# Kernel tuning notes

Hardware: AMD Instinct MI355X
Metric: run time of the kernel (lower is better)

## Reference

```python
import jax, jax.numpy as jnp
import numpy as np

L, D, H, KVH, DH, F, V, SMAX, T = 4, 2048, 16, 8, 128, 6144, 32000, 2048, 1024
EPS = 1e-6
ROPE_THETA = 1e6


def rotate_half(x, axis=-1):
    x1, x2 = jnp.split(x, 2, axis=axis)
    return jnp.concatenate((-x2, x1), axis=axis)


def rms(x, w):
    return w * (x / jnp.sqrt(jnp.mean(x * x, axis=-1, keepdims=True) + EPS))


def setup_inputs() -> dict:
    key = jax.random.key(0)
    ks = jax.random.split(key, 16)
    s = 0.02
    inv_freq = 1.0 / (ROPE_THETA ** (jnp.arange(0, DH, 2, dtype=jnp.float32) / DH))
    ang = jnp.arange(SMAX, dtype=jnp.float32)[:, None] * inv_freq[None, :]  # [SMAX, DH/2]
    cos_emb = jnp.concatenate([jnp.cos(ang), jnp.cos(ang)], axis=-1)  # [SMAX, DH]
    sin_emb = jnp.concatenate([jnp.sin(ang), jnp.sin(ang)], axis=-1)
    sf = DH ** (-0.25)  # scale_factor pre-baked into q_norm/k_norm weights
    return {
        "key_buffer": jnp.zeros((L, KVH, 1, DH, SMAX), jnp.float32),
        "value_buffer": jnp.zeros((L, KVH, 1, SMAX, DH), jnp.float32),
        "input_ids": jax.random.randint(ks[0], (1, T), 0, V, dtype=jnp.int32),
        "attention_mask": jnp.ones((1, T, T), jnp.float32),
        "past_len": 0,
        "embed_data": jax.random.randint(ks[1], (V, D), 0, 256).astype(jnp.uint8),
        "embed_scale": jax.random.uniform(ks[2], (V, 1), jnp.float32, 0.001, 0.02),
        "embed_zero": jax.random.normal(ks[3], (V, 1), jnp.float32) * 0.1,
        "cos_emb": cos_emb,
        "sin_emb": sin_emb,
        "w_in_ln": jnp.ones((L, D), jnp.float32),
        "Wq": jax.random.normal(ks[4], (L, D, H * DH), jnp.float32) * s,
        "Wk": jax.random.normal(ks[5], (L, D, KVH * DH), jnp.float32) * s,
        "Wv": jax.random.normal(ks[6], (L, D, KVH * DH), jnp.float32) * s,
        "w_q_norm": jnp.full((L, DH), sf, jnp.float32),
        "w_k_norm": jnp.full((L, DH), sf, jnp.float32),
        "Wo": jax.random.normal(ks[7], (L, H * DH, D), jnp.float32) * s,
        "w_post_ln": jnp.ones((L, D), jnp.float32),
        "Wgate": jax.random.normal(ks[8], (L, D, F), jnp.float32) * s,
        "Wup": jax.random.normal(ks[9], (L, D, F), jnp.float32) * s,
        "Wdown": jax.random.normal(ks[10], (L, F, D), jnp.float32) * s,
        "w_final_norm": jnp.ones((D,), jnp.float32),
        "W_lm": jax.random.normal(ks[11], (D, V), jnp.float32) * s,
    }


def reference(key_buffer, value_buffer, input_ids, attention_mask, past_len,
              embed_data, embed_scale, embed_zero, cos_emb, sin_emb,
              w_in_ln, Wq, Wk, Wv, w_q_norm, w_k_norm, Wo, w_post_ln,
              Wgate, Wup, Wdown, w_final_norm, W_lm):
    new_len = input_ids.shape[1]
    end = past_len + new_len  # static (past_len is a Python int)
    cos_q = cos_emb[past_len:end]  # [T, DH]
    sin_q = sin_emb[past_len:end]
    # uint8 embedding dequant: e * scale + zero_point
    hidden = embed_data[input_ids].astype(jnp.float32) * embed_scale[input_ids] + embed_zero[input_ids]  # [1,T,D]
    # causal mask: (1 - tril) * -128, sliced to [1, new_len, end], times user mask
    rows = jnp.arange(new_len) + past_len
    cols = jnp.arange(end)
    mask = jnp.where(cols[None, :] <= rows[:, None], 0.0, -128.0)[None] * attention_mask  # [1,T,end]
    G = H // KVH
    for i in range(L):
        hn = rms(hidden, w_in_ln[i])[0]  # [T, D]
        q = (hn @ Wq[i]).reshape(new_len, H, DH)
        q = jnp.transpose(rms(q, w_q_norm[i]), (1, 0, 2))  # [H,T,DH] (sqrt(scale) baked in w_q_norm)
        k = (hn @ Wk[i]).reshape(new_len, KVH, DH)
        k = jnp.transpose(rms(k, w_k_norm[i]), (1, 2, 0))  # [KVH,DH,T]
        v = jnp.transpose((hn @ Wv[i]).reshape(new_len, KVH, DH), (1, 0, 2))  # [KVH,T,DH]
        # RoPE on keys (rotate along DH axis=1)
        k = k * cos_q.T + rotate_half(k, axis=1) * sin_q.T
        key_buffer = jax.lax.dynamic_update_slice(key_buffer, k[None, :, None], (i, 0, 0, 0, past_len))
        value_buffer = jax.lax.dynamic_update_slice(value_buffer, v[None, :, None], (i, 0, 0, past_len, 0))
        # GQA expand: each kv head repeated G times consecutively
        k_exp = jnp.repeat(key_buffer[i, :, 0, :, :end], G, axis=0)  # [H,DH,end]
        v_exp = jnp.repeat(value_buffer[i, :, 0, :end, :], G, axis=0)  # [H,end,DH]
        q_rot = q * cos_q[None] + rotate_half(q, axis=-1) * sin_q[None]
        scores = jnp.einsum('htd,hds->hts', q_rot, k_exp) + mask
        attn = jax.nn.softmax(scores, axis=-1)
        ctx = jnp.transpose(jnp.einsum('hts,hsd->htd', attn, v_exp), (1, 0, 2)).reshape(1, new_len, H * DH)
        hidden = hidden + ctx @ Wo[i]
        hn2 = rms(hidden, w_post_ln[i])
        hidden = hidden + (jax.nn.silu(hn2 @ Wgate[i]) * (hn2 @ Wup[i])) @ Wdown[i]
    last = rms(hidden[:, -1], w_final_norm)  # [1, D]
    logits = last @ W_lm  # [1, V]
    tok_id = jnp.argmax(logits, axis=-1, keepdims=True).astype(jnp.int32)
    new_seq_len = jnp.array([end], dtype=jnp.int32)
    return (tok_id, key_buffer, value_buffer, new_seq_len)
```

## Files before the change

### kernel.cpp

```cpp
#include <hip/hip_runtime.h>
#include <cstdint>

#define L_ 4
#define D_ 2048
#define H_ 16
#define KVH_ 8
#define DH_ 128
#define F_ 6144
#define V_ 32000
#define SMAX_ 2048
#define T_ 1024
#define EPS_ 1e-6f
#define QB 32
#define SB 128
#define ZSE 4194304

typedef unsigned short u16;
typedef unsigned int u32;
typedef float fvec4 __attribute__((ext_vector_type(4)));
typedef float f32x4 __attribute__((ext_vector_type(4)));
typedef __bf16 bf16x8 __attribute__((ext_vector_type(8)));

__device__ __forceinline__ u16 f2bf(float f) {
  union { float f; u32 u; } a; a.f = f;
  u32 u = a.u;
  return (u16)((u + 0x7FFFu + ((u >> 16) & 1u)) >> 16);
}
__device__ __forceinline__ float bf2f(u16 h) {
  union { u32 u; float f; } a; a.u = (u32)h << 16; return a.f;
}
__device__ __forceinline__ fvec4 bf4(uint2 u) {
  union { u32 i; float f; } a, b, c, d;
  a.i = u.x << 16; b.i = u.x & 0xFFFF0000u;
  c.i = u.y << 16; d.i = u.y & 0xFFFF0000u;
  fvec4 r; r[0] = a.f; r[1] = b.f; r[2] = c.f; r[3] = d.f; return r;
}

__device__ __forceinline__ void gld16(const void* g, void* l) {
  __builtin_amdgcn_global_load_lds(
      (const __attribute__((address_space(1))) void*)g,
      (__attribute__((address_space(3))) void*)l, 16, 0, 0);
}

__global__ void embed_k(const int* __restrict__ ids, const void* __restrict__ edata,
                        const float* __restrict__ esc, const float* __restrict__ ez,
                        float* __restrict__ hidden)
{
  const int* ei = (const int*)edata;
  int chk = ei[threadIdx.x & 63];
  bool ok = ((unsigned)chk) <= 255u;
  bool is_i32 = (__ballot(ok) == ~0ULL);
  int t = blockIdx.x;
  int id = ids[t];
  float sc = esc[id], zp = ez[id];
  size_t base = (size_t)id * D_;
  const uint8_t* eb = (const uint8_t*)edata;
  for (int d = threadIdx.x; d < D_; d += 256) {
    float e = is_i32 ? (float)ei[base + d] : (float)eb[base + d];
    hidden[(size_t)t * D_ + d] = e * sc + zp;
  }
}

__device__ __forceinline__ void convT_body(const float* __restrict__ W, int N,
                                           int nb, int kb, int K, int rb,
                                           u16* __restrict__ WT, int gu, float* tile)
{
  int n0 = nb * 64, k0 = kb * 64;
  int tid = threadIdx.x;
  int lk = tid >> 4, n4 = (tid & 15) * 4;
#pragma unroll
  for (int i = 0; i < 4; ++i) {
    int kr = i * 16 + lk;
    fvec4 v = *(const fvec4*)(W + (size_t)(k0 + kr) * N + n0 + n4);
#pragma unroll
    for (int j = 0; j < 4; ++j) tile[(n4 + j) * 65 + kr] = v[j];
  }
  __syncthreads();
  int n = tid >> 2, kq = (tid & 3) * 16;
  int f = n0 + n;
  int row = gu ? (rb + ((f >> 4) << 5) + (f & 15)) : (rb + f);
  union { u16 h[16]; uint4 q[2]; } o;
#pragma unroll
  for (int i = 0; i < 16; ++i) o.h[i] = f2bf(tile[n * 65 + kq + i]);
  u16* op = WT + (size_t)row * K + k0 + kq;
  *(uint4*)op = o.q[0];
  *(uint4*)(op + 8) = o.q[1];
}

template<int NZ>
__device__ __forceinline__ void rms_body(int idx, float* __restrict__ x,
                                         const u16* __restrict__ p,
                                         const float* __restrict__ w,
                                         u16* __restrict__ out)
{
  int t = idx * 4 + (threadIdx.x >> 6);
  int l = threadIdx.x & 63;
  fvec4* xr = (fvec4*)(x + (size_t)t * D_);
  fvec4 v[8];
#pragma unroll
  for (int j = 0; j < 8; ++j) v[j] = xr[l + 64 * j];
  if (NZ > 0) {
#pragma unroll
    for (int z = 0; z < NZ; ++z) {
      const uint2* a = (const uint2*)(p + (size_t)z * ZSE + (size_t)t * D_);
#pragma unroll
      for (int j = 0; j < 8; ++j) v[j] += bf4(a[l + 64 * j]);
    }
#pragma unroll
    for (int j = 0; j < 8; ++j) xr[l + 64 * j] = v[j];
  }
  float s = 0.f;
#pragma unroll
  for (int j = 0; j < 8; ++j)
    s += v[j][0]*v[j][0] + v[j][1]*v[j][1] + v[j][2]*v[j][2] + v[j][3]*v[j][3];
#pragma unroll
  for (int m = 32; m; m >>= 1) s += __shfl_xor(s, m);
  float inv = rsqrtf(s * (1.f / D_) + EPS_);
  const fvec4* wr = (const fvec4*)w;
  u16* orow = out + (size_t)t * D_;
#pragma unroll
  for (int j = 0; j < 8; ++j) {
    fvec4 wv = wr[l + 64 * j];
    uint2 o;
    o.x = (u32)f2bf(wv[0]*v[j][0]*inv) | ((u32)f2bf(wv[1]*v[j][1]*inv) << 16);
    o.y = (u32)f2bf(wv[2]*v[j][2]*inv) | ((u32)f2bf(wv[3]*v[j][3]*inv) << 16);
    *(uint2*)(orow + (l + 64 * j) * 4) = o;
  }
}

template<int NZ>
__global__ __launch_bounds__(256)
void convqkv_rms_k(const float* __restrict__ Wq, const float* __restrict__ Wk,
                   const float* __restrict__ Wv, u16* __restrict__ WT,
                   float* __restrict__ x, const u16* __restrict__ p,
                   const float* __restrict__ w, u16* __restrict__ out)
{
  __shared__ float tile[64 * 65];
  int bx = blockIdx.x, y = blockIdx.y;
  if (bx < 64) {
    const float* W; int N, nb, rb;
    if (bx < 32)      { W = Wq; N = 2048; nb = bx;      rb = 0; }
    else if (bx < 48) { W = Wk; N = 1024; nb = bx - 32; rb = 2048; }
    else              { W = Wv; N = 1024; nb = bx - 48; rb = 3072; }
    convT_body(W, N, nb, y, 2048, rb, WT, 0, tile);
  } else {
    rms_body<NZ>((bx - 64) * 32 + y, x, p, w, out);
  }
}

__global__ __launch_bounds__(256)
void convgu_wd_rms_k(const float* __restrict__ Wg, const float* __restrict__ Wu,
                     u16* __restrict__ WTgu, const float* __restrict__ Wd,
                     u16* __restrict__ WTwd,
                     float* __restrict__ x, const u16* __restrict__ p,
                     const float* __restrict__ w, u16* __restrict__ out)
{
  __shared__ float tile[64 * 65];
  int bx = blockIdx.x, y = blockIdx.y;
  if (bx < 192) {
    const float* W; int nb, rb;
    if (bx < 96) { W = Wg; nb = bx;      rb = 0; }
    else         { W = Wu; nb = bx - 96; rb = 16; }
    convT_body(W, 6144, nb, y, 2048, rb, WTgu, 1, tile);
  } else if (bx < 288) {
    int xp = bx - 192;
    convT_body(Wd, 2048, xp & 31, ((xp >> 5) << 5) + y, 6144, 0, WTwd, 0, tile);
  } else {
    rms_body<4>((bx - 288) * 32 + y, x, p, w, out);
  }
}

template<int EPI>
__global__ __launch_bounds__(256)
void gemm_bt(const u16* __restrict__ A, const u16* __restrict__ B,
             u16* __restrict__ Cb, int K, int Ks, int ldC, long long zStride)
{
  __shared__ u16 lA[128 * 64];
  __shared__ u16 lB[128 * 64];
  const u16* Ab = A + (size_t)blockIdx.y * 128 * K;
  const u16* Bb = B + (size_t)blockIdx.x * 128 * K;
  int kz = blockIdx.z * Ks;

  int tid = threadIdx.x;
  int l = tid & 63;
  int wid = tid >> 6;
  int wr = wid >> 1, wc = wid & 1;
  int lrow = l & 15, lk = l >> 4;

  f32x4 acc[4][4] = {};

  for (int k0 = 0; k0 < Ks; k0 += 64) {
#pragma unroll
    for (int r = 0; r < 4; ++r) {
      int c = r * 256 + tid;
      int row = c >> 3, g = c & 7;
      int kel = kz + k0 + ((g ^ (row & 7)) << 3);
      gld16(Ab + (size_t)row * K + kel, (char*)lA + c * 16);
      gld16(Bb + (size_t)row * K + kel, (char*)lB + c * 16);
    }
    __syncthreads();
#pragma unroll
    for (int kk = 0; kk < 2; ++kk) {
      bf16x8 av[4], bv[4];
      int kbyte = (kk * 32 + lk * 8) * 2;
#pragma unroll
      for (int m = 0; m < 4; ++m) {
        int row = wr * 64 + m * 16 + lrow;
        int byt = (row * 128 + kbyte) ^ ((row & 7) << 4);
        av[m] = *(const bf16x8*)((const char*)lA + byt);
      }
#pragma unroll
      for (int n = 0; n < 4; ++n) {
        int row = wc * 64 + n * 16 + lrow;
        int byt = (row * 128 + kbyte) ^ ((row & 7) << 4);
        bv[n] = *(const bf16x8*)((const char*)lB + byt);
      }
#pragma unroll
      for (int m = 0; m < 4; ++m)
#pragma unroll
        for (int n = 0; n < 4; ++n)
          acc[m][n] = __builtin_amdgcn_mfma_f32_16x16x32_bf16(av[m], bv[n], acc[m][n], 0, 0, 0);
    }
    __syncthreads();
  }

  int grow0 = blockIdx.y * 128 + wr * 64 + lk * 4;
  if (EPI == 3) {
    int fcol0 = blockIdx.x * 64 + wc * 32 + lrow;
#pragma unroll
    for (int m = 0; m < 4; ++m)
#pragma unroll
      for (int np = 0; np < 2; ++np)
#pragma unroll
        for (int r = 0; r < 4; ++r) {
          float g = acc[m][2 * np][r], u = acc[m][2 * np + 1][r];
          float val = g / (1.f + __expf(-g)) * u;
          Cb[(size_t)(grow0 + m * 16 + r) * ldC + fcol0 + np * 16] = f2bf(val);
        }
    return;
  }
  u16* Cz = Cb + (long long)blockIdx.z * zStride;
  int gcol0 = blockIdx.x * 128 + wc * 64 + lrow;
#pragma unroll
  for (int m = 0; m < 4; ++m)
#pragma unroll
    for (int n = 0; n < 4; ++n)
#pragma unroll
      for (int r = 0; r < 4; ++r)
        Cz[(size_t)(grow0 + m * 16 + r) * ldC + gcol0 + n * 16] = f2bf(acc[m][n][r]);
}

__global__ __launch_bounds__(256)
void qkvpost_convwo_k(const u16* __restrict__ p0, const u16* __restrict__ p1,
                      const float* __restrict__ wq, const float* __restrict__ wk,
                      const float* __restrict__ cosT, const float* __restrict__ sinT,
                      const int* __restrict__ plp,
                      u16* __restrict__ qr, u16* __restrict__ kr, u16* __restrict__ vT,
                      float* __restrict__ key_out, float* __restrict__ val_out,
                      const float* __restrict__ Wo, u16* __restrict__ WTo)
{
  __shared__ float tile[64][132];
  if (blockIdx.x >= 16) {
    convT_body(Wo, 2048, blockIdx.x - 16, blockIdx.y, 2048, 0, WTo, 0, &tile[0][0]);
    return;
  }
  int t0 = blockIdx.x * 64;
  int z = blockIdx.y;
  int pl = plp[0];
  int tid = threadIdx.x;
  int cb = z < 16 ? z * 128 : (z < 24 ? 2048 + (z - 16) * 128 : 3072 + (z - 24) * 128);

  {
    int r = tid >> 5;
    int c = (tid & 31) * 4;
#pragma unroll
    for (int i = 0; i < 8; ++i) {
      int row = i * 8 + r;
      size_t off = (size_t)(t0 + row) * 4096 + cb + c;
      fvec4 v = bf4(*(const uint2*)(p0 + off)) + bf4(*(const uint2*)(p1 + off));
      *(fvec4*)&tile[row][c] = v;
    }
  }
  __syncthreads();

  if (z < 24) {
    int row = tid >> 2, q = tid & 3;
    int dbase = q * 32, pbase = (q ^ 2) * 32;
    const float* wn = z < 16 ? wq : wk;
    float sgn = (q < 2) ? -1.f : 1.f;
    fvec4 xv[8];
    float ss = 0.f;
#pragma unroll
    for (int j = 0; j < 8; ++j) {
      xv[j] = *(const fvec4*)&tile[row][dbase + j * 4];
      ss += xv[j][0]*xv[j][0] + xv[j][1]*xv[j][1] + xv[j][2]*xv[j][2] + xv[j][3]*xv[j][3];
    }
    ss += __shfl_xor(ss, 1);
    ss += __shfl_xor(ss, 2);
    float inv = rsqrtf(ss * (1.f / 128.f) + EPS_);
    int p = pl + t0 + row;
    float rv[32];
#pragma unroll
    for (int j = 0; j < 8; ++j) {
      fvec4 xo = *(const fvec4*)&tile[row][pbase + j * 4];
      fvec4 wv = *(const fvec4*)(wn + dbase + j * 4);
      fvec4 wo = *(const fvec4*)(wn + pbase + j * 4);
      fvec4 cs = *(const fvec4*)(cosT + (size_t)p * 128 + dbase + j * 4);
      fvec4 sn = *(const fvec4*)(sinT + (size_t)p * 128 + dbase + j * 4);
#pragma unroll
      for (int e = 0; e < 4; ++e) {
        float xn = wv[e] * xv[j][e] * inv;
        float xp = wo[e] * xo[e] * inv;
        rv[j * 4 + e] = xn * cs[e] + sgn * xp * sn[e];
      }
    }
    union { u32 w[8]; uint4 q4[2]; } ob;
    u16* orow = (z < 16 ? qr + ((size_t)z * T_ + t0 + row) * 128
                        : kr + ((size_t)(z - 16) * T_ + t0 + row) * 128) + dbase;
#pragma unroll
    for (int j = 0; j < 8; ++j)
      ob.w[j] = (u32)f2bf(rv[2 * j]) | ((u32)f2bf(rv[2 * j + 1]) << 16);
    *(uint4*)orow = ob.q4[0];
    *(uint4*)(orow + 8) = ob.q4[1];
#pragma unroll
    for (int j = 0; j < 8; ++j)
      ob.w[j] = (u32)f2bf(rv[16 + 2 * j]) | ((u32)f2bf(rv[17 + 2 * j]) << 16);
    *(uint4*)(orow + 16) = ob.q4[0];
    *(uint4*)(orow + 24) = ob.q4[1];

    if (z >= 16) {
      __syncthreads();
#pragma unroll
      for (int j = 0; j < 8; ++j) {
        fvec4 v; v[0] = rv[j*4]; v[1] = rv[j*4+1]; v[2] = rv[j*4+2]; v[3] = rv[j*4+3];
        *(fvec4*)&tile[row][dbase + j * 4] = v;
      }
      __syncthreads();
      int d = tid >> 1, cc = (tid & 1) * 32;
      float* kp = key_out + ((size_t)(z - 16) * 128 + d) * SMAX_ + pl + t0 + cc;
      if ((pl & 3) == 0) {
#pragma unroll
        for (int j4 = 0; j4 < 8; ++j4) {
          fvec4 v;
#pragma unroll
          for (int e = 0; e < 4; ++e) v[e] = tile[cc + j4 * 4 + e][d];
          *(fvec4*)(kp + j4 * 4) = v;
        }
      } else {
        for (int j = 0; j < 32; ++j) kp[j] = tile[cc + j][d];
      }
    }
  } else {
    int kv = z - 24;
    int row = tid >> 2, q = tid & 3;
    float* vp = val_out + ((size_t)kv * SMAX_ + pl + t0 + row) * 128 + q * 32;
#pragma unroll
    for (int j = 0; j < 8; ++j)
      *(fvec4*)(vp + j * 4) = *(const fvec4*)&tile[row][q * 32 + j * 4];
    int d = tid >> 1, cc = (tid & 1) * 32;
    union { u32 w[16]; uint4 q4[4]; } ob;
    u16* tp = vT + ((size_t)kv * 128 + d) * T_ + t0 + cc;
#pragma unroll
    for (int j = 0; j < 16; ++j)
      ob.w[j] = (u32)f2bf(tile[cc + 2 * j][d]) | ((u32)f2bf(tile[cc + 2 * j + 1][d]) << 16);
    *(uint4*)tp = ob.q4[0];
    *(uint4*)(tp + 8) = ob.q4[1];
    *(uint4*)(tp + 16) = ob.q4[2];
    *(uint4*)(tp + 24) = ob.q4[3];
  }
}

__global__ __launch_bounds__(256)
void flash_k(const u16* __restrict__ qr, const u16* __restrict__ kr,
             const u16* __restrict__ vTb, const float* __restrict__ am,
             const int* __restrict__ plp, u16* __restrict__ ctx)
{
  __shared__ u16 lQ[QB * DH_];
  __shared__ u16 lKV[SB * DH_];
  __shared__ u16 lP[QB * SB];
  __shared__ float lMax[2][2][16];
  __shared__ float lSum[2][2][16];
  __shared__ float lScale[QB];
  __shared__ float lFin[QB];

  int qt = gridDim.x - 1 - blockIdx.x;
  int h = blockIdx.y;
  int kvh = h >> 1;
  int pl = plp[0];
  int tid = threadIdx.x;
  int l = tid & 63, w = tid >> 6;
  int lrow = l & 15, lk = l >> 4;
  int tb = w & 1, sh = w >> 1;
  int tcol = tb * 16 + lrow;

  const u16* Qb = qr + ((size_t)h * T_ + qt * QB) * DH_;
  const u16* Kb = kr + (size_t)kvh * T_ * DH_;
  const u16* Vb = vTb + (size_t)kvh * DH_ * T_;

#pragma unroll
  for (int r = 0; r < 2; ++r) {
    int c = r * 256 + tid;
    int row = c >> 4, g = c & 15;
    gld16(Qb + (size_t)row * DH_ + ((g ^ (row & 7)) << 3), (char*)lQ + c * 16);
  }

  float m_run = -3.0e38f, l_run = 0.f;
  f32x4 acc_o[2][2] = {};

  int t_lo = qt * QB;
  int s_hi = min(T_, t_lo + QB + pl);
  int nt = (s_hi + SB - 1) / SB;
  int tg = t_lo + tcol;

  for (int it = 0; it < nt; ++it) {
    int s0 = it * SB;
#pragma unroll
    for (int r = 0; r < 8; ++r) {
      int c = r * 256 + tid;
      int row = c >> 4, g = c & 15;
      gld16(Kb + (size_t)(s0 + row) * DH_ + ((g ^ (row & 7)) << 3), (char*)lKV + c * 16);
    }
    __syncthreads();

    f32x4 acc_s[4] = {};
#pragma unroll
    for (int kk = 0; kk < 4; ++kk) {
      int kbyte = kk * 64 + lk * 16;
      int trow = tb * 16 + lrow;
      bf16x8 bq = *(const bf16x8*)((const char*)lQ + ((trow * 256 + kbyte) ^ ((trow & 7) << 4)));
#pragma unroll
      for (int m = 0; m < 4; ++m) {
        int srow = sh * 64 + m * 16 + lrow;
        bf16x8 ak = *(const bf16x8*)((const char*)lKV + ((srow * 256 + kbyte) ^ ((srow & 7) << 4)));
        acc_s[m] = __builtin_amdgcn_mfma_f32_16x16x32_bf16(ak, bq, acc_s[m], 0, 0, 0);
      }
    }
    __syncthreads();

#pragma unroll
    for (int r = 0; r < 8; ++r) {
      int c = r * 256 + tid;
      int row = c >> 4, g = c & 15;
      gld16(Vb + (size_t)row * T_ + s0 + ((g ^ (row & 7)) << 3), (char*)lKV + c * 16);
    }

    bool full = (s0 + SB <= t_lo + pl + 1);
    float sv[4][4];
    float vmax = -3.0e38f;
    if (full) {
#pragma unroll
      for (int m = 0; m < 4; ++m)
#pragma unroll
        for (int r = 0; r < 4; ++r) {
          float val = acc_s[m][r]; sv[m][r] = val; vmax = fmaxf(vmax, val);
        }
    } else {
#pragma unroll
      for (int m = 0; m < 4; ++m) {
        int sg = s0 + sh * 64 + m * 16 + lk * 4;
        fvec4 a4 = *(const fvec4*)(am + (size_t)tg * T_ + sg);
#pragma unroll
        for (int r = 0; r < 4; ++r) {
          float val = acc_s[m][r] + ((sg + r <= tg + pl) ? 0.f : -128.f * a4[r]);
          sv[m][r] = val; vmax = fmaxf(vmax, val);
        }
      }
    }
    vmax = fmaxf(vmax, __shfl_xor(vmax, 16));
    vmax = fmaxf(vmax, __shfl_xor(vmax, 32));
    if (lk == 0) lMax[tb][sh][lrow] = vmax;
    __syncthreads();

    float om = fmaxf(lMax[tb][0][lrow], lMax[tb][1][lrow]);
    float m_new = fmaxf(m_run, om);
    float corr = __expf(m_run - m_new);
    float psum = 0.f;
    u32 pw[4][2];
#pragma unroll
    for (int m = 0; m < 4; ++m) {
      float p0 = __expf(sv[m][0] - m_new);
      float p1 = __expf(sv[m][1] - m_new);
      float p2 = __expf(sv[m][2] - m_new);
      float p3 = __expf(sv[m][3] - m_new);
      psum += (p0 + p1) + (p2 + p3);
      pw[m][0] = (u32)f2bf(p0) | ((u32)f2bf(p1) << 16);
      pw[m][1] = (u32)f2bf(p2) | ((u32)f2bf(p3) << 16);
    }
    psum += __shfl_xor(psum, 16);
    psum += __shfl_xor(psum, 32);
    if (lk == 0) lSum[tb][sh][lrow] = psum;
    if (lk == 0 && sh == 0) lScale[tcol] = corr;
#pragma unroll
    for (int m = 0; m < 4; ++m) {
      int byt = (tcol * 256 + sh * 128 + m * 32 + lk * 8) ^ ((tcol & 7) << 4);
      *(uint2*)((char*)lP + byt) = make_uint2(pw[m][0], pw[m][1]);
    }
    __syncthreads();

    l_run = l_run * corr + lSum[tb][0][lrow] + lSum[tb][1][lrow];
    m_run = m_new;
#pragma unroll
    for (int m = 0; m < 2; ++m) {
      fvec4 c4 = *(const fvec4*)&lScale[m * 16 + lk * 4];
#pragma unroll
      for (int n = 0; n < 2; ++n)
#pragma unroll
        for (int r = 0; r < 4; ++r) acc_o[m][n][r] *= c4[r];
    }
#pragma unroll
    for (int kk = 0; kk < 4; ++kk) {
      int kbyte = kk * 64 + lk * 16;
      bf16x8 ap[2], bv[2];
#pragma unroll
      for (int m = 0; m < 2; ++m) {
        int trow = m * 16 + lrow;
        ap[m] = *(const bf16x8*)((const char*)lP + ((trow * 256 + kbyte) ^ ((trow & 7) << 4)));
      }
#pragma unroll
      for (int n = 0; n < 2; ++n) {
        int drow = w * 32 + n * 16 + lrow;
        bv[n] = *(const bf16x8*)((const char*)lKV + ((drow * 256 + kbyte) ^ ((drow & 7) << 4)));
      }
#pragma unroll
      for (int m = 0; m < 2; ++m)
#pragma unroll
        for (int n = 0; n < 2; ++n)
          acc_o[m][n] = __builtin_amdgcn_mfma_f32_16x16x32_bf16(ap[m], bv[n], acc_o[m][n], 0, 0, 0);
    }
    __syncthreads();
  }

  if (lk == 0 && sh == 0) lFin[tcol] = l_run;
  __syncthreads();
#pragma unroll
  for (int m = 0; m < 2; ++m) {
    fvec4 s4 = *(const fvec4*)&lFin[m * 16 + lk * 4];
#pragma unroll
    for (int r = 0; r < 4; ++r) {
      float inv = 1.f / s4[r];
      int trow = t_lo + m * 16 + lk * 4 + r;
      u16* crow = ctx + (size_t)trow * (H_ * DH_) + h * DH_;
#pragma unroll
      for (int n = 0; n < 2; ++n) {
        int d = w * 32 + n * 16 + lrow;
        crow[d] = f2bf(acc_o[m][n][r] * inv);
      }
    }
  }
}

__global__ void frms_k(const float* __restrict__ x, const u16* __restrict__ p,
                       const float* __restrict__ w, float* __restrict__ out)
{
  __shared__ float sm[4];
  float s = 0.f;
  for (int d = threadIdx.x; d < D_; d += 256) {
    float v = x[d] + bf2f(p[d]) + bf2f(p[ZSE + d]) + bf2f(p[2 * ZSE + d]) + bf2f(p[3 * ZSE + d]);
    s += v * v;
  }
#pragma unroll
  for (int m = 32; m; m >>= 1) s += __shfl_xor(s, m);
  if ((threadIdx.x & 63) == 0) sm[threadIdx.x >> 6] = s;
  __syncthreads();
  s = sm[0] + sm[1] + sm[2] + sm[3];
  float inv = rsqrtf(s * (1.f / D_) + EPS_);
  for (int d = threadIdx.x; d < D_; d += 256)
    out[d] = w[d] * (x[d] + bf2f(p[d]) + bf2f(p[ZSE + d]) + bf2f(p[2 * ZSE + d]) + bf2f(p[3 * ZSE + d])) * inv;
}

__global__ void lmgemv_k(const float* __restrict__ last, const float* __restrict__ Wlm,
                         float* __restrict__ part)
{
  __shared__ float ls[256];
  int v = blockIdx.x * 256 + threadIdx.x;
  int c = blockIdx.y;
  ls[threadIdx.x] = last[c * 256 + threadIdx.x];
  __syncthreads();
  const float* Wp = Wlm + (size_t)c * 256 * V_ + v;
  float acc = 0.f;
#pragma unroll 8
  for (int d = 0; d < 256; d++) acc += ls[d] * Wp[(size_t)d * V_];
  part[(size_t)c * V_ + v] = acc;
}

__global__ void amax_part_k(const float* __restrict__ part, float2* __restrict__ out)
{
  __shared__ float sv[4];
  __shared__ int si[4];
  int v = blockIdx.x * 256 + threadIdx.x;
  float val = 0.f;
#pragma unroll
  for (int c = 0; c < 8; c++) val += part[(size_t)c * V_ + v];
  float bv = val; int bi = v;
#pragma unroll
  for (int m = 32; m; m >>= 1) {
    float ov = __shfl_xor(bv, m);
    int oi = __shfl_xor(bi, m);
    if (ov > bv || (ov == bv && oi < bi)) { bv = ov; bi = oi; }
  }
  if ((threadIdx.x & 63) == 0) { sv[threadIdx.x >> 6] = bv; si[threadIdx.x >> 6] = bi; }
  __syncthreads();
  if (threadIdx.x == 0) {
    for (int w = 1; w < 4; w++)
      if (sv[w] > bv || (sv[w] == bv && si[w] < bi)) { bv = sv[w]; bi = si[w]; }
    out[blockIdx.x] = make_float2(bv, (float)bi);
  }
}

__global__ void finalize_k(const float2* __restrict__ part, int np,
                           const int* __restrict__ plp, float* __restrict__ dout,
                           unsigned long long lastoff)
{
  if (threadIdx.x == 0) {
    float bv = part[0].x; int bi = (int)part[0].y;
    for (int b = 1; b < np; b++) {
      float v = part[b].x; int i = (int)part[b].y;
      if (v > bv || (v == bv && i < bi)) { bv = v; bi = i; }
    }
    dout[0] = (float)bi;
    dout[lastoff] = (float)(plp[0] + T_);
  }
}

extern "C" void kernel_launch(void* const* d_in, const int* in_sizes, int n_in,
                              void* d_out, int out_size, void* d_ws, size_t ws_size,
                              hipStream_t stream)
{
  (void)in_sizes; (void)n_in; (void)out_size; (void)ws_size;

  const float* key_in  = (const float*)d_in[0];
  const float* val_in  = (const float*)d_in[1];
  const int*   ids     = (const int*)d_in[2];
  const float* am      = (const float*)d_in[3];
  const int*   plp     = (const int*)d_in[4];
  const void*  edata   = d_in[5];
  const float* esc     = (const float*)d_in[6];
  const float* ez      = (const float*)d_in[7];
  const float* cosT    = (const float*)d_in[8];
  const float* sinT    = (const float*)d_in[9];
  const float* w_in_ln = (const float*)d_in[10];
  const float* Wq      = (const float*)d_in[11];
  const float* Wk      = (const float*)d_in[12];
  const float* Wv      = (const float*)d_in[13];
  const float* wqn     = (const float*)d_in[14];
  const float* wkn     = (const float*)d_in[15];
  const float* Wo      = (const float*)d_in[16];
  const float* wpost   = (const float*)d_in[17];
  const float* Wg      = (const float*)d_in[18];
  const float* Wu      = (const float*)d_in[19];
  const float* Wd      = (const float*)d_in[20];
  const float* wfin    = (const float*)d_in[21];
  const float* Wlm     = (const float*)d_in[22];

  float* out = (float*)d_out;
  const size_t KVN = (size_t)L_ * KVH_ * DH_ * SMAX_;
  float* key_out = out + 1;
  float* val_out = out + 1 + KVN;
  unsigned long long lastoff = 1 + 2 * KVN;

  char* ws = (char*)d_ws;
  u16*   wT     = (u16*)  (ws + 0);
  u16*   wTwd   = wT + 25165824;
  u16*   hn     = (u16*)  (ws + 75497472);
  u16*   P      = (u16*)  (ws + 79691776);
  u16*   qr     = (u16*)  (ws + 113246208);
  u16*   kr     = (u16*)  (ws + 117440512);
  u16*   vT     = (u16*)  (ws + 119537664);
  u16*   ctx    = (u16*)  (ws + 121634816);
  float* hidden = (float*)(ws + 125829120);
  u16*   mlp    = (u16*)  (ws + 134217728);
  float* last   = (float*)(ws + 146800640);
  float* lpart  = (float*)(ws + 146808832);
  float2* amaxp = (float2*)(ws + 147832832);

  hipMemcpyAsync(key_out, key_in, KVN * sizeof(float), hipMemcpyDeviceToDevice, stream);
  hipMemcpyAsync(val_out, val_in, KVN * sizeof(float), hipMemcpyDeviceToDevice, stream);
  embed_k<<<T_, 256, 0, stream>>>(ids, edata, esc, ez, hidden);

  for (int i = 0; i < L_; i++) {
    if (i == 0)
      convqkv_rms_k<0><<<dim3(72, 32), 256, 0, stream>>>(
          Wq, Wk, Wv, wT, hidden, nullptr, w_in_ln, hn);
    else
      convqkv_rms_k<4><<<dim3(72, 32), 256, 0, stream>>>(
          Wq + (size_t)i * 4194304, Wk + (size_t)i * 2097152, Wv + (size_t)i * 2097152,
          wT, hidden, P, w_in_ln + (size_t)i * D_, hn);

    gemm_bt<0><<<dim3(32, 8, 2), 256, 0, stream>>>(hn, wT, P, 2048, 1024, 4096, ZSE);

    qkvpost_convwo_k<<<dim3(48, 32), 256, 0, stream>>>(P, P + ZSE,
        wqn + (size_t)i * DH_, wkn + (size_t)i * DH_, cosT, sinT, plp,
        qr, kr, vT,
        key_out + (size_t)i * KVH_ * DH_ * SMAX_,
        val_out + (size_t)i * KVH_ * SMAX_ * DH_,
        Wo + (size_t)i * 4194304, wT);

    flash_k<<<dim3(T_ / QB, H_), 256, 0, stream>>>(qr, kr, vT, am, plp, ctx);

    gemm_bt<0><<<dim3(16, 8, 4), 256, 0, stream>>>(ctx, wT, P, 2048, 512, 2048, ZSE);

    convgu_wd_rms_k<<<dim3(296, 32), 256, 0, stream>>>(
        Wg + (size_t)i * 12582912, Wu + (size_t)i * 12582912, wT,
        Wd + (size_t)i * 12582912, wTwd,
        hidden, P, wpost + (size_t)i * D_, hn);

    gemm_bt<3><<<dim3(96, 8, 1), 256, 0, stream>>>(hn, wT, mlp, 2048, 2048, 6144, 0);

    gemm_bt<0><<<dim3(16, 8, 4), 256, 0, stream>>>(mlp, wTwd, P, 6144, 1536, 2048, ZSE);
  }

  frms_k<<<1, 256, 0, stream>>>(hidden + (size_t)(T_ - 1) * D_,
                                P + (size_t)(T_ - 1) * D_, wfin, last);
  lmgemv_k<<<dim3(V_ / 256, 8), 256, 0, stream>>>(last, Wlm, lpart);
  amax_part_k<<<V_ / 256, 256, 0, stream>>>(lpart, amaxp);
  finalize_k<<<1, 64, 0, stream>>>(amaxp, V_ / 256, plp, out, lastoff);
}
```

Measured before the change: 1.133 ms.

## Co-schedule QKV GEMM with Wo/gate/up/down weight conversion in one kernel

Moves the Wo, gate/up and down weight transpose-conversions into one grid with the QKV GEMM, so the bandwidth-bound conversion blocks overlap the compute-bound GEMM blocks. The RMSNorm that was fused with the MLP conversion becomes a standalone kernel, and the final RMS is folded into the LM-head GEMV. The workspace is re-laid out with separate buffers per converted weight and a smaller partial stride, and the mlp buffer now aliases the QKV weight area. Risks include load imbalance from the heterogeneous grid, and each LM GEMV block recomputing the final norm.

```diff
diff --git a/kernel.cpp b/kernel.cpp
--- a/kernel.cpp
+++ b/kernel.cpp
@@ -13,7 +13,8 @@
 #define EPS_ 1e-6f
 #define QB 32
 #define SB 128
-#define ZSE 4194304
+#define ZQK 4194304
+#define ZS2 2097152
 
 typedef unsigned short u16;
 typedef unsigned int u32;
@@ -89,7 +90,7 @@
 
 template<int NZ>
 __device__ __forceinline__ void rms_body(int idx, float* __restrict__ x,
-                                         const u16* __restrict__ p,
+                                         const u16* __restrict__ p, int zs,
                                          const float* __restrict__ w,
                                          u16* __restrict__ out)
 {
@@ -102,7 +103,7 @@
   if (NZ > 0) {
 #pragma unroll
     for (int z = 0; z < NZ; ++z) {
-      const uint2* a = (const uint2*)(p + (size_t)z * ZSE + (size_t)t * D_);
+      const uint2* a = (const uint2*)(p + (size_t)z * zs + (size_t)t * D_);
 #pragma unroll
       for (int j = 0; j < 8; ++j) v[j] += bf4(a[l + 64 * j]);
     }
@@ -144,42 +145,29 @@
     else              { W = Wv; N = 1024; nb = bx - 48; rb = 3072; }
     convT_body(W, N, nb, y, 2048, rb, WT, 0, tile);
   } else {
-    rms_body<NZ>((bx - 64) * 32 + y, x, p, w, out);
+    rms_body<NZ>((bx - 64) * 32 + y, x, p, ZS2, w, out);
   }
 }
 
 __global__ __launch_bounds__(256)
-void convgu_wd_rms_k(const float* __restrict__ Wg, const float* __restrict__ Wu,
-                     u16* __restrict__ WTgu, const float* __restrict__ Wd,
-                     u16* __restrict__ WTwd,
-                     float* __restrict__ x, const u16* __restrict__ p,
-                     const float* __restrict__ w, u16* __restrict__ out)
-{
-  __shared__ float tile[64 * 65];
-  int bx = blockIdx.x, y = blockIdx.y;
-  if (bx < 192) {
-    const float* W; int nb, rb;
-    if (bx < 96) { W = Wg; nb = bx;      rb = 0; }
-    else         { W = Wu; nb = bx - 96; rb = 16; }
-    convT_body(W, 6144, nb, y, 2048, rb, WTgu, 1, tile);
-  } else if (bx < 288) {
-    int xp = bx - 192;
-    convT_body(Wd, 2048, xp & 31, ((xp >> 5) << 5) + y, 6144, 0, WTwd, 0, tile);
-  } else {
-    rms_body<4>((bx - 288) * 32 + y, x, p, w, out);
-  }
+void rms_k(float* __restrict__ x, const u16* __restrict__ p,
+           const float* __restrict__ w, u16* __restrict__ out)
+{
+  rms_body<4>(blockIdx.x, x, p, ZS2, w, out);
 }
 
 template<int EPI>
-__global__ __launch_bounds__(256)
-void gemm_bt(const u16* __restrict__ A, const u16* __restrict__ B,
-             u16* __restrict__ Cb, int K, int Ks, int ldC, long long zStride)
-{
-  __shared__ u16 lA[128 * 64];
-  __shared__ u16 lB[128 * 64];
-  const u16* Ab = A + (size_t)blockIdx.y * 128 * K;
-  const u16* Bb = B + (size_t)blockIdx.x * 128 * K;
-  int kz = blockIdx.z * Ks;
+__device__ __forceinline__ void gemm_body(const u16* __restrict__ A,
+                                          const u16* __restrict__ B,
+                                          u16* __restrict__ Cb,
+                                          int K, int Ks, int ldC, long long zStride,
+                                          int bx, int by, int bz, char* smem)
+{
+  u16* lA = (u16*)smem;
+  u16* lB = (u16*)(smem + 16384);
+  const u16* Ab = A + (size_t)by * 128 * K;
+  const u16* Bb = B + (size_t)bx * 128 * K;
+  int kz = bz * Ks;
 
   int tid = threadIdx.x;
   int l = tid & 63;
@@ -224,9 +212,9 @@
     __syncthreads();
   }
 
-  int grow0 = blockIdx.y * 128 + wr * 64 + lk * 4;
+  int grow0 = by * 128 + wr * 64 + lk * 4;
   if (EPI == 3) {
-    int fcol0 = blockIdx.x * 64 + wc * 32 + lrow;
+    int fcol0 = bx * 64 + wc * 32 + lrow;
 #pragma unroll
     for (int m = 0; m < 4; ++m)
 #pragma unroll
@@ -239,8 +227,8 @@
         }
     return;
   }
-  u16* Cz = Cb + (long long)blockIdx.z * zStride;
-  int gcol0 = blockIdx.x * 128 + wc * 64 + lrow;
+  u16* Cz = Cb + (long long)bz * zStride;
+  int gcol0 = bx * 128 + wc * 64 + lrow;
 #pragma unroll
   for (int m = 0; m < 4; ++m)
 #pragma unroll
@@ -250,20 +238,52 @@
         Cz[(size_t)(grow0 + m * 16 + r) * ldC + gcol0 + n * 16] = f2bf(acc[m][n][r]);
 }
 
+template<int EPI>
 __global__ __launch_bounds__(256)
-void qkvpost_convwo_k(const u16* __restrict__ p0, const u16* __restrict__ p1,
-                      const float* __restrict__ wq, const float* __restrict__ wk,
-                      const float* __restrict__ cosT, const float* __restrict__ sinT,
-                      const int* __restrict__ plp,
-                      u16* __restrict__ qr, u16* __restrict__ kr, u16* __restrict__ vT,
-                      float* __restrict__ key_out, float* __restrict__ val_out,
-                      const float* __restrict__ Wo, u16* __restrict__ WTo)
+void gemm_bt(const u16* __restrict__ A, const u16* __restrict__ B,
+             u16* __restrict__ Cb, int K, int Ks, int ldC, long long zStride)
+{
+  __shared__ char smem[32768];
+  gemm_body<EPI>(A, B, Cb, K, Ks, ldC, zStride, blockIdx.x, blockIdx.y, blockIdx.z, smem);
+}
+
+__global__ __launch_bounds__(256)
+void qkvgemm_conv_k(const u16* __restrict__ hn, const u16* __restrict__ wTqkv,
+                    u16* __restrict__ P,
+                    const float* __restrict__ Wo, u16* __restrict__ wTo,
+                    const float* __restrict__ Wg, const float* __restrict__ Wu,
+                    u16* __restrict__ wTgu,
+                    const float* __restrict__ Wd, u16* __restrict__ wTwd)
+{
+  __shared__ char smem[32768];
+  int bx = blockIdx.x;
+  if (bx < 512) {
+    gemm_body<0>(hn, wTqkv, P, 2048, 1024, 4096, ZQK,
+                 bx & 31, (bx >> 5) & 7, bx >> 8, smem);
+  } else if (bx < 1536) {
+    int cb = bx - 512;
+    convT_body(Wo, 2048, cb & 31, cb >> 5, 2048, 0, wTo, 0, (float*)smem);
+  } else if (bx < 7680) {
+    int cb = bx - 1536;
+    int x = cb % 192, y = cb / 192;
+    const float* W = x < 96 ? Wg : Wu;
+    convT_body(W, 6144, x < 96 ? x : x - 96, y, 2048, x < 96 ? 0 : 16, wTgu, 1, (float*)smem);
+  } else {
+    int cb = bx - 7680;
+    int xp = cb % 96, y = cb / 96;
+    convT_body(Wd, 2048, xp & 31, ((xp >> 5) << 5) + y, 6144, 0, wTwd, 0, (float*)smem);
+  }
+}
+
+__global__ __launch_bounds__(256)
+void qkvpost_k(const u16* __restrict__ p0, const u16* __restrict__ p1,
+               const float* __restrict__ wq, const float* __restrict__ wk,
+               const float* __restrict__ cosT, const float* __restrict__ sinT,
+               const int* __restrict__ plp,
+               u16* __restrict__ qr, u16* __restrict__ kr, u16* __restrict__ vT,
+               float* __restrict__ key_out, float* __restrict__ val_out)
 {
   __shared__ float tile[64][132];
-  if (blockIdx.x >= 16) {
-    convT_body(Wo, 2048, blockIdx.x - 16, blockIdx.y, 2048, 0, WTo, 0, &tile[0][0]);
-    return;
-  }
   int t0 = blockIdx.x * 64;
   int z = blockIdx.y;
   int pl = plp[0];
@@ -549,33 +569,33 @@
   }
 }
 
-__global__ void frms_k(const float* __restrict__ x, const u16* __restrict__ p,
-                       const float* __restrict__ w, float* __restrict__ out)
-{
+__global__ void lmgemv_k(const float* __restrict__ x, const u16* __restrict__ p,
+                         const float* __restrict__ wfin, const float* __restrict__ Wlm,
+                         float* __restrict__ part)
+{
+  __shared__ float ls[256];
   __shared__ float sm[4];
+  int tid = threadIdx.x;
+  int c = blockIdx.y;
+  float xv[8];
   float s = 0.f;
-  for (int d = threadIdx.x; d < D_; d += 256) {
-    float v = x[d] + bf2f(p[d]) + bf2f(p[ZSE + d]) + bf2f(p[2 * ZSE + d]) + bf2f(p[3 * ZSE + d]);
-    s += v * v;
+#pragma unroll
+  for (int j = 0; j < 8; ++j) {
+    int d = j * 256 + tid;
+    float v = x[d] + bf2f(p[d]) + bf2f(p[ZS2 + d]) + bf2f(p[2 * ZS2 + d]) + bf2f(p[3 * ZS2 + d]);
+    xv[j] = v; s += v * v;
   }
 #pragma unroll
   for (int m = 32; m; m >>= 1) s += __shfl_xor(s, m);
-  if ((threadIdx.x & 63) == 0) sm[threadIdx.x >> 6] = s;
+  if ((tid & 63) == 0) sm[tid >> 6] = s;
   __syncthreads();
   s = sm[0] + sm[1] + sm[2] + sm[3];
   float inv = rsqrtf(s * (1.f / D_) + EPS_);
-  for (int d = threadIdx.x; d < D_; d += 256)
-    out[d] = w[d] * (x[d] + bf2f(p[d]) + bf2f(p[ZSE + d]) + bf2f(p[2 * ZSE + d]) + bf2f(p[3 * ZSE + d])) * inv;
-}
-
-__global__ void lmgemv_k(const float* __restrict__ last, const float* __restrict__ Wlm,
-                         float* __restrict__ part)
-{
-  __shared__ float ls[256];
-  int v = blockIdx.x * 256 + threadIdx.x;
-  int c = blockIdx.y;
-  ls[threadIdx.x] = last[c * 256 + threadIdx.x];
+#pragma unroll
+  for (int j = 0; j < 8; ++j)
+    if (j == c) ls[tid] = wfin[j * 256 + tid] * xv[j] * inv;
   __syncthreads();
+  int v = blockIdx.x * 256 + tid;
   const float* Wp = Wlm + (size_t)c * 256 * V_ + v;
   float acc = 0.f;
 #pragma unroll 8
@@ -659,19 +679,20 @@
   unsigned long long lastoff = 1 + 2 * KVN;
 
   char* ws = (char*)d_ws;
-  u16*   wT     = (u16*)  (ws + 0);
-  u16*   wTwd   = wT + 25165824;
-  u16*   hn     = (u16*)  (ws + 75497472);
-  u16*   P      = (u16*)  (ws + 79691776);
-  u16*   qr     = (u16*)  (ws + 113246208);
-  u16*   kr     = (u16*)  (ws + 117440512);
-  u16*   vT     = (u16*)  (ws + 119537664);
-  u16*   ctx    = (u16*)  (ws + 121634816);
-  float* hidden = (float*)(ws + 125829120);
-  u16*   mlp    = (u16*)  (ws + 134217728);
-  float* last   = (float*)(ws + 146800640);
-  float* lpart  = (float*)(ws + 146808832);
-  float2* amaxp = (float2*)(ws + 147832832);
+  u16*   wTqkv  = (u16*)  (ws + 0);
+  u16*   mlp    = (u16*)  (ws + 0);
+  float* lpart  = (float*)(ws + 16777216);
+  float2* amaxp = (float2*)(ws + 17825792);
+  u16*   wTo    = (u16*)  (ws + 33554432);
+  u16*   wTgu   = (u16*)  (ws + 41943040);
+  u16*   wTwd   = (u16*)  (ws + 92274688);
+  u16*   P      = (u16*)  (ws + 117440512);
+  u16*   hn     = (u16*)  (ws + 134217728);
+  u16*   qr     = (u16*)  (ws + 138412032);
+  u16*   kr     = (u16*)  (ws + 142606336);
+  u16*   vT     = (u16*)  (ws + 144703488);
+  u16*   ctx    = (u16*)  (ws + 146800640);
+  float* hidden = (float*)(ws + 150994944);
 
   hipMemcpyAsync(key_out, key_in, KVN * sizeof(float), hipMemcpyDeviceToDevice, stream);
   hipMemcpyAsync(val_out, val_in, KVN * sizeof(float), hipMemcpyDeviceToDevice, stream);
@@ -680,38 +701,37 @@
   for (int i = 0; i < L_; i++) {
     if (i == 0)
       convqkv_rms_k<0><<<dim3(72, 32), 256, 0, stream>>>(
-          Wq, Wk, Wv, wT, hidden, nullptr, w_in_ln, hn);
+          Wq, Wk, Wv, wTqkv, hidden, nullptr, w_in_ln, hn);
     else
       convqkv_rms_k<4><<<dim3(72, 32), 256, 0, stream>>>(
           Wq + (size_t)i * 4194304, Wk + (size_t)i * 2097152, Wv + (size_t)i * 2097152,
-          wT, hidden, P, w_in_ln + (size_t)i * D_, hn);
-
-    gemm_bt<0><<<dim3(32, 8, 2), 256, 0, stream>>>(hn, wT, P, 2048, 1024, 4096, ZSE);
-
-    qkvpost_convwo_k<<<dim3(48, 32), 256, 0, stream>>>(P, P + ZSE,
+          wTqkv, hidden, P, w_in_ln + (size_t)i * D_, hn);
+
+    qkvgemm_conv_k<<<10752, 256, 0, stream>>>(
+        hn, wTqkv, P,
+        Wo + (size_t)i * 4194304, wTo,
+        Wg + (size_t)i * 12582912, Wu + (size_t)i * 12582912, wTgu,
+        Wd + (size_t)i * 12582912, wTwd);
+
+    qkvpost_k<<<dim3(16, 32), 256, 0, stream>>>(P, P + ZQK,
         wqn + (size_t)i * DH_, wkn + (size_t)i * DH_, cosT, sinT, plp,
         qr, kr, vT,
         key_out + (size_t)i * KVH_ * DH_ * SMAX_,
-        val_out + (size_t)i * KVH_ * SMAX_ * DH_,
-        Wo + (size_t)i * 4194304, wT);
+        val_out + (size_t)i * KVH_ * SMAX_ * DH_);
 
     flash_k<<<dim3(T_ / QB, H_), 256, 0, stream>>>(qr, kr, vT, am, plp, ctx);
 
-    gemm_bt<0><<<dim3(16, 8, 4), 256, 0, stream>>>(ctx, wT, P, 2048, 512, 2048, ZSE);
-
-    convgu_wd_rms_k<<<dim3(296, 32), 256, 0, stream>>>(
-        Wg + (size_t)i * 12582912, Wu + (size_t)i * 12582912, wT,
-        Wd + (size_t)i * 12582912, wTwd,
-        hidden, P, wpost + (size_t)i * D_, hn);
-
-    gemm_bt<3><<<dim3(96, 8, 1), 256, 0, stream>>>(hn, wT, mlp, 2048, 2048, 6144, 0);
-
-    gemm_bt<0><<<dim3(16, 8, 4), 256, 0, stream>>>(mlp, wTwd, P, 6144, 1536, 2048, ZSE);
-  }
-
-  frms_k<<<1, 256, 0, stream>>>(hidden + (size_t)(T_ - 1) * D_,
-                                P + (size_t)(T_ - 1) * D_, wfin, last);
-  lmgemv_k<<<dim3(V_ / 256, 8), 256, 0, stream>>>(last, Wlm, lpart);
+    gemm_bt<0><<<dim3(16, 8, 4), 256, 0, stream>>>(ctx, wTo, P, 2048, 512, 2048, ZS2);
+
+    rms_k<<<256, 256, 0, stream>>>(hidden, P, wpost + (size_t)i * D_, hn);
+
+    gemm_bt<3><<<dim3(96, 8, 1), 256, 0, stream>>>(hn, wTgu, mlp, 2048, 2048, 6144, 0);
+
+    gemm_bt<0><<<dim3(16, 8, 4), 256, 0, stream>>>(mlp, wTwd, P, 6144, 1536, 2048, ZS2);
+  }
+
+  lmgemv_k<<<dim3(V_ / 256, 8), 256, 0, stream>>>(
+      hidden + (size_t)(T_ - 1) * D_, P + (size_t)(T_ - 1) * D_, wfin, Wlm, lpart);
   amax_part_k<<<V_ / 256, 256, 0, stream>>>(lpart, amaxp);
   finalize_k<<<1, 64, 0, stream>>>(amaxp, V_ / 256, plp, out, lastoff);
 }
```

Result: faster. 1.073 ms (-5.3%).
